# Optimization experiments

Hardware: AMD Instinct MI355X
Metric: run time of the kernel (lower is better)

The kernel has to match this reference:

```python
import jax, jax.numpy as jnp
import numpy as np
from jax import lax

RATIO = 4
NUM_UPS = 2  # log2(RATIO)

def _taps():
    cdf23 = 2.0 * np.array([0.5, 0.305334091185, 0.0, -0.072698593239, 0.0,
                            0.021809577942, 0.0, -0.005192756653, 0.0,
                            0.000807762146, 0.0, -6.0081482e-05])
    base = np.concatenate([cdf23[1:][::-1], cdf23])  # 23 symmetric taps
    return jnp.asarray(base, dtype=jnp.float32)

def _dwconv(x, kern, c):
    # depthwise cross-correlation, matches torch F.conv2d(groups=c)
    return lax.conv_general_dilated(
        x, kern, window_strides=(1, 1), padding='VALID',
        dimension_numbers=('NCHW', 'OIHW', 'NCHW'), feature_group_count=c)

def setup_inputs() -> dict:
    key = jax.random.key(0)
    x = jax.random.normal(key, (16, 8, 160, 160), dtype=jnp.float32)
    return {"x": x}

def reference(x) -> jnp.ndarray:
    taps = _taps()                      # [23]
    pad = (taps.shape[0] - 1) // 2      # 11
    bs, c, h, w = x.shape
    kw = jnp.tile(taps.reshape(1, 1, 1, -1), (c, 1, 1, 1))  # [c,1,1,23]
    kh = jnp.tile(taps.reshape(1, 1, -1, 1), (c, 1, 1, 1))  # [c,1,23,1]
    cur = x
    for k in range(NUM_UPS):
        h, w = h * 2, w * 2
        off = 1 if k == 0 else 0
        up = jnp.zeros((bs, c, h, w), dtype=x.dtype)
        up = up.at[..., off::2, off::2].set(cur)  # zero-insertion upsample
        # width pass: replicate pad + 1x23 depthwise conv
        pw = jnp.pad(up, ((0, 0), (0, 0), (0, 0), (pad, pad)), mode='edge')
        fw = _dwconv(pw, kw, c)
        # height pass: circular pad + 23x1 depthwise conv
        ph = jnp.pad(fw, ((0, 0), (0, 0), (pad, pad), (0, 0)), mode='wrap')
        cur = _dwconv(ph, kh, c)
    return cur
```

## Files before the change

kernel.cpp:

```cpp
#include <hip/hip_runtime.h>

typedef float v4f __attribute__((ext_vector_type(4)));

constexpr float W12c[12] = {
    -1.20162964e-04f,    1.615524292e-03f, -1.0385513306e-02f,  4.3619155884e-02f,
    -1.45397186478e-01f, 6.1066818237e-01f, 6.1066818237e-01f, -1.45397186478e-01f,
     4.3619155884e-02f, -1.0385513306e-02f, 1.615524292e-03f,  -1.20162964e-04f
};

struct GTabs { float ge[17]; float go[17]; };
constexpr GTabs make_gtabs() {
    GTabs t{};
    for (int d = 0; d < 17; ++d) { t.ge[d] = 0.f; t.go[d] = 0.f; }
    for (int v = 0; v < 6; ++v) { t.ge[v + 5] += W12c[2 * v]; t.go[v + 6] += W12c[2 * v + 1]; }
    for (int v = 0; v < 6; ++v)
        for (int u = 0; u < 12; ++u) {
            t.ge[v + u] += W12c[2 * v + 1] * W12c[u];
            t.go[v + u] += W12c[2 * v]     * W12c[u];
        }
    return t;
}
__device__ constexpr GTabs G = make_gtabs();

__device__ __forceinline__ int xcd_map(int bid, int nblk) {
    int cpx = nblk >> 3;
    return (bid & 7) * cpx + (bid >> 3);
}

__global__ __launch_bounds__(256) void k_fused(const float* __restrict__ x,
                                               float* __restrict__ out) {
    __shared__ float ww[48][132];

    int bid = xcd_map(blockIdx.x, gridDim.x);
    int ct = bid % 5, rt = (bid / 5) % 5, bc = bid / 25;
    int KQ = rt * 32;
    int MC0 = ct * 64;
    int WB = KQ - 8;
    int tid = threadIdx.x;

#pragma unroll
    for (int it = 0; it < 2; ++it) {
        int idx = it * 256 + tid;
        if (idx < 384) {
            int e = idx >> 3, g = idx & 7;
            int m = WB + e; m = m < 0 ? m + 160 : (m >= 160 ? m - 160 : m);
            const float* xr = x + (bc * 160 + m) * 160;
            int XC0 = 32 * ct + 4 * g - 8;
            int qb0 = (32 * ct + 4 * g - 8) >> 2;
            float flat[20];
#pragma unroll
            for (int b = 0; b < 5; ++b) {
                int bq = qb0 + b; bq = bq < 0 ? 0 : (bq > 39 ? 39 : bq);
                *(v4f*)(flat + 4 * b) = *(const v4f*)(xr + 4 * bq);
            }
            if (ct == 0 && g < 2) {
#pragma unroll
                for (int p = 0; p < 8; ++p) flat[p] = (XC0 + p < 0) ? 0.f : flat[p];
            }
            float x159 = flat[19];
            if (ct == 4 && g >= 6) {
#pragma unroll
                for (int p = 12; p < 20; ++p) flat[p] = (XC0 + p > 159) ? x159 : flat[p];
            }
            float mcol[19];
#pragma unroll
            for (int t = 0; t < 9; ++t) {
                float acc = 0.f;
#pragma unroll
                for (int s = 0; s < 12; ++s) acc += W12c[s] * flat[t + s];
                mcol[2 * t + 1] = acc;
            }
#pragma unroll
            for (int t = 0; t < 10; ++t) mcol[2 * t] = flat[5 + t];
            if (ct == 4 && g >= 5) {
#pragma unroll
                for (int t = 0; t < 10; ++t) {
                    int xi = XC0 + 5 + t;
                    float c = 0.f;
#pragma unroll
                    for (int s = 0; s < 12; ++s) if (xi + s >= 165) c += W12c[s];
                    mcol[2 * t] += c * x159;
                }
            }
            float mid0 = mcol[5];
            if (ct == 0 && g == 0) {
#pragma unroll
                for (int p = 0; p < 5; ++p) mcol[p] = mid0;
            }
            if (ct == 4 && g == 7) {
#pragma unroll
                for (int p = 13; p < 19; ++p) mcol[p] = 0.f;
            }
            float oe[8], oo[8];
#pragma unroll
            for (int d = 0; d < 8; ++d) {
                float acc = 0.f;
#pragma unroll
                for (int s = 0; s < 12; ++s) acc += W12c[s] * mcol[d + s];
                oo[d] = acc;
                oe[d] = mcol[d + 5];
            }
            if (ct == 0 && g == 0) {
#pragma unroll
                for (int d = 0; d < 6; ++d) {
                    float c = 0.f;
#pragma unroll
                    for (int s = 0; s < 12; ++s) if (d + s <= 5) c += W12c[s];
                    oe[d] += c * mid0;
                }
            }
#pragma unroll
            for (int j = 0; j < 4; ++j) {
                v4f v;
                v.x = oe[2 * j];     v.y = oo[2 * j];
                v.z = oe[2 * j + 1]; v.w = oo[2 * j + 1];
                *(v4f*)(&ww[e][16 * g + 4 * j]) = v;
            }
        }
    }
    __syncthreads();

    {
        int c4 = tid & 31, slot = tid >> 5;
        float* dbase = out + (size_t)bc * 640 * 640 + 2 * MC0 + 4 * c4;
        int eb = slot * 4;
        v4f w[17];
#pragma unroll
        for (int t = 0; t < 17; ++t) w[t] = *(const v4f*)(&ww[eb + t][4 * c4]);
#pragma unroll
        for (int q = 0; q < 4; ++q) {
            if (q > 0) {
#pragma unroll
                for (int t = 0; t < 16; ++t) w[t] = w[t + 1];
                w[16] = *(const v4f*)(&ww[eb + q + 16][4 * c4]);
            }
            int k = KQ + eb + q;
            float* r0 = dbase + (size_t)(4 * k) * 640;
            v4f a = W12c[0] * w[2];
#pragma unroll
            for (int u = 1; u < 12; ++u) a += W12c[u] * w[u + 2];
            *(v4f*)(r0) = a;
            v4f b = G.ge[0] * w[0];
#pragma unroll
            for (int d = 1; d < 17; ++d) b += G.ge[d] * w[d];
            *(v4f*)(r0 + 640) = b;
            *(v4f*)(r0 + 1280) = w[8];
            v4f c = G.go[0] * w[0];
#pragma unroll
            for (int d = 1; d < 17; ++d) c += G.go[d] * w[d];
            *(v4f*)(r0 + 1920) = c;
        }
    }
}

extern "C" void kernel_launch(void* const* d_in, const int* in_sizes, int n_in,
                              void* d_out, int out_size, void* d_ws, size_t ws_size,
                              hipStream_t stream) {
    const float* x = (const float*)d_in[0];
    float* out = (float*)d_out;
    k_fused<<<3200, 256, 0, stream>>>(x, out);
}
```

Measured before the change: 40.91 us.

## Split shared tile generation to overlap second-half producer with first-half output

Tile generation now runs in two phases. All 256 threads first build rows 0-31 of the intermediate tile in shared memory. After a barrier, threads 0-127 build rows 32-47 while every thread emits the first half of the output quads, which only need rows 0-31. A second barrier then precedes the second half of the emit. This removes the old pattern where half the threads sat idle during the second generation pass before any stores could start. The cost is an extra barrier and warp imbalance during the overlapped phase, and the kernel is likely bound by output writes anyway.

```diff
diff --git a/kernel.cpp b/kernel.cpp
--- a/kernel.cpp
+++ b/kernel.cpp
@@ -38,118 +38,129 @@
     int WB = KQ - 8;
     int tid = threadIdx.x;
 
+    auto gen_ww = [&](int e, int g) {
+        int m = WB + e; m = m < 0 ? m + 160 : (m >= 160 ? m - 160 : m);
+        const float* xr = x + (bc * 160 + m) * 160;
+        int XC0 = 32 * ct + 4 * g - 8;
+        int qb0 = XC0 >> 2;
+        float flat[20];
 #pragma unroll
-    for (int it = 0; it < 2; ++it) {
-        int idx = it * 256 + tid;
-        if (idx < 384) {
-            int e = idx >> 3, g = idx & 7;
-            int m = WB + e; m = m < 0 ? m + 160 : (m >= 160 ? m - 160 : m);
-            const float* xr = x + (bc * 160 + m) * 160;
-            int XC0 = 32 * ct + 4 * g - 8;
-            int qb0 = (32 * ct + 4 * g - 8) >> 2;
-            float flat[20];
+        for (int b = 0; b < 5; ++b) {
+            int bq = qb0 + b; bq = bq < 0 ? 0 : (bq > 39 ? 39 : bq);
+            *(v4f*)(flat + 4 * b) = *(const v4f*)(xr + 4 * bq);
+        }
+        if (ct == 0 && g < 2) {
 #pragma unroll
-            for (int b = 0; b < 5; ++b) {
-                int bq = qb0 + b; bq = bq < 0 ? 0 : (bq > 39 ? 39 : bq);
-                *(v4f*)(flat + 4 * b) = *(const v4f*)(xr + 4 * bq);
-            }
-            if (ct == 0 && g < 2) {
+            for (int p = 0; p < 8; ++p) flat[p] = (XC0 + p < 0) ? 0.f : flat[p];
+        }
+        float x159 = flat[19];
+        if (ct == 4 && g >= 6) {
 #pragma unroll
-                for (int p = 0; p < 8; ++p) flat[p] = (XC0 + p < 0) ? 0.f : flat[p];
-            }
-            float x159 = flat[19];
-            if (ct == 4 && g >= 6) {
+            for (int p = 12; p < 20; ++p) flat[p] = (XC0 + p > 159) ? x159 : flat[p];
+        }
+        float mcol[19];
 #pragma unroll
-                for (int p = 12; p < 20; ++p) flat[p] = (XC0 + p > 159) ? x159 : flat[p];
-            }
-            float mcol[19];
+        for (int t = 0; t < 9; ++t) {
+            float acc = 0.f;
 #pragma unroll
-            for (int t = 0; t < 9; ++t) {
-                float acc = 0.f;
+            for (int s = 0; s < 12; ++s) acc += W12c[s] * flat[t + s];
+            mcol[2 * t + 1] = acc;
+        }
 #pragma unroll
-                for (int s = 0; s < 12; ++s) acc += W12c[s] * flat[t + s];
-                mcol[2 * t + 1] = acc;
-            }
+        for (int t = 0; t < 10; ++t) mcol[2 * t] = flat[5 + t];
+        if (ct == 4 && g >= 5) {
 #pragma unroll
-            for (int t = 0; t < 10; ++t) mcol[2 * t] = flat[5 + t];
-            if (ct == 4 && g >= 5) {
+            for (int t = 0; t < 10; ++t) {
+                int xi = XC0 + 5 + t;
+                float c = 0.f;
 #pragma unroll
-                for (int t = 0; t < 10; ++t) {
-                    int xi = XC0 + 5 + t;
-                    float c = 0.f;
-#pragma unroll
-                    for (int s = 0; s < 12; ++s) if (xi + s >= 165) c += W12c[s];
-                    mcol[2 * t] += c * x159;
-                }
-            }
-            float mid0 = mcol[5];
-            if (ct == 0 && g == 0) {
-#pragma unroll
-                for (int p = 0; p < 5; ++p) mcol[p] = mid0;
-            }
-            if (ct == 4 && g == 7) {
-#pragma unroll
-                for (int p = 13; p < 19; ++p) mcol[p] = 0.f;
-            }
-            float oe[8], oo[8];
-#pragma unroll
-            for (int d = 0; d < 8; ++d) {
-                float acc = 0.f;
-#pragma unroll
-                for (int s = 0; s < 12; ++s) acc += W12c[s] * mcol[d + s];
-                oo[d] = acc;
-                oe[d] = mcol[d + 5];
-            }
-            if (ct == 0 && g == 0) {
-#pragma unroll
-                for (int d = 0; d < 6; ++d) {
-                    float c = 0.f;
-#pragma unroll
-                    for (int s = 0; s < 12; ++s) if (d + s <= 5) c += W12c[s];
-                    oe[d] += c * mid0;
-                }
-            }
-#pragma unroll
-            for (int j = 0; j < 4; ++j) {
-                v4f v;
-                v.x = oe[2 * j];     v.y = oo[2 * j];
-                v.z = oe[2 * j + 1]; v.w = oo[2 * j + 1];
-                *(v4f*)(&ww[e][16 * g + 4 * j]) = v;
+                for (int s = 0; s < 12; ++s) if (xi + s >= 165) c += W12c[s];
+                mcol[2 * t] += c * x159;
             }
         }
+        float mid0 = mcol[5];
+        if (ct == 0 && g == 0) {
+#pragma unroll
+            for (int p = 0; p < 5; ++p) mcol[p] = mid0;
+        }
+        if (ct == 4 && g == 7) {
+#pragma unroll
+            for (int p = 13; p < 19; ++p) mcol[p] = 0.f;
+        }
+        float oe[8], oo[8];
+#pragma unroll
+        for (int d = 0; d < 8; ++d) {
+            float acc = 0.f;
+#pragma unroll
+            for (int s = 0; s < 12; ++s) acc += W12c[s] * mcol[d + s];
+            oo[d] = acc;
+            oe[d] = mcol[d + 5];
+        }
+        if (ct == 0 && g == 0) {
+#pragma unroll
+            for (int d = 0; d < 6; ++d) {
+                float c = 0.f;
+#pragma unroll
+                for (int s = 0; s < 12; ++s) if (d + s <= 5) c += W12c[s];
+                oe[d] += c * mid0;
+            }
+        }
+#pragma unroll
+        for (int j = 0; j < 4; ++j) {
+            v4f v;
+            v.x = oe[2 * j];     v.y = oo[2 * j];
+            v.z = oe[2 * j + 1]; v.w = oo[2 * j + 1];
+            *(v4f*)(&ww[e][16 * g + 4 * j]) = v;
+        }
+    };
+
+    int c4 = tid & 31, slot = tid >> 5;
+    float* dbase = out + (size_t)bc * 640 * 640 + 2 * MC0 + 4 * c4;
+    auto emit_quad = [&](const v4f* w, int kk) {
+        int k = KQ + kk;
+        float* r0 = dbase + (size_t)(4 * k) * 640;
+        v4f a = W12c[0] * w[2];
+#pragma unroll
+        for (int u = 1; u < 12; ++u) a += W12c[u] * w[u + 2];
+        *(v4f*)(r0) = a;
+        v4f b = G.ge[0] * w[0];
+#pragma unroll
+        for (int d = 1; d < 17; ++d) b += G.ge[d] * w[d];
+        *(v4f*)(r0 + 640) = b;
+        *(v4f*)(r0 + 1280) = w[8];
+        v4f c = G.go[0] * w[0];
+#pragma unroll
+        for (int d = 1; d < 17; ++d) c += G.go[d] * w[d];
+        *(v4f*)(r0 + 1920) = c;
+    };
+
+    gen_ww(tid >> 3, tid & 7);
+    __syncthreads();
+
+    if (tid < 128) {
+        gen_ww(32 + (tid >> 3), tid & 7);
+    }
+    {
+        v4f w[17];
+#pragma unroll
+        for (int t = 0; t < 17; ++t) w[t] = *(const v4f*)(&ww[2 * slot + t][4 * c4]);
+        emit_quad(w, 2 * slot);
+#pragma unroll
+        for (int t = 0; t < 16; ++t) w[t] = w[t + 1];
+        w[16] = *(const v4f*)(&ww[2 * slot + 17][4 * c4]);
+        emit_quad(w, 2 * slot + 1);
     }
     __syncthreads();
 
     {
-        int c4 = tid & 31, slot = tid >> 5;
-        float* dbase = out + (size_t)bc * 640 * 640 + 2 * MC0 + 4 * c4;
-        int eb = slot * 4;
         v4f w[17];
 #pragma unroll
-        for (int t = 0; t < 17; ++t) w[t] = *(const v4f*)(&ww[eb + t][4 * c4]);
+        for (int t = 0; t < 17; ++t) w[t] = *(const v4f*)(&ww[16 + 2 * slot + t][4 * c4]);
+        emit_quad(w, 16 + 2 * slot);
 #pragma unroll
-        for (int q = 0; q < 4; ++q) {
-            if (q > 0) {
-#pragma unroll
-                for (int t = 0; t < 16; ++t) w[t] = w[t + 1];
-                w[16] = *(const v4f*)(&ww[eb + q + 16][4 * c4]);
-            }
-            int k = KQ + eb + q;
-            float* r0 = dbase + (size_t)(4 * k) * 640;
-            v4f a = W12c[0] * w[2];
-#pragma unroll
-            for (int u = 1; u < 12; ++u) a += W12c[u] * w[u + 2];
-            *(v4f*)(r0) = a;
-            v4f b = G.ge[0] * w[0];
-#pragma unroll
-            for (int d = 1; d < 17; ++d) b += G.ge[d] * w[d];
-            *(v4f*)(r0 + 640) = b;
-            *(v4f*)(r0 + 1280) = w[8];
-            v4f c = G.go[0] * w[0];
-#pragma unroll
-            for (int d = 1; d < 17; ++d) c += G.go[d] * w[d];
-            *(v4f*)(r0 + 1920) = c;
-        }
+        for (int t = 0; t < 16; ++t) w[t] = w[t + 1];
+        w[16] = *(const v4f*)(&ww[16 + 2 * slot + 17][4 * c4]);
+        emit_quad(w, 16 + 2 * slot + 1);
     }
 }
 
```

After: 41.43 us. About the same (+1.3%).
